# Optimization experiments

Hardware: AMD Instinct MI355X
Metric: run time of the kernel (lower is better)

## Reference

```python
import jax, jax.numpy as jnp
import numpy as np

ORDER = 3  # polynomial filter order


def _sketch_conv(x, A, W, b, coeffs):
    # z = A @ (x W + b); out = sum_d coeffs[d-1] * z**d  (Horner-free power accumulation)
    z = A @ (x @ W + b)            # [N, out_c]
    p = z
    acc = coeffs[0] * z
    for d in range(1, ORDER):      # small fixed loop over polynomial order
        p = p * z
        acc = acc + coeffs[d] * p
    return acc


def setup_inputs() -> dict:
    key = jax.random.key(0)
    ks = jax.random.split(key, 12)
    N, C_IN, C_H, C_OUT = 8192, 128, 64, 40
    nf_mats = jax.random.normal(ks[0], (N, C_IN), dtype=jnp.float32)
    # scale by 1/sqrt(N) so polynomial powers stay O(1)
    conv_mats = jax.random.normal(ks[1], (N, N), dtype=jnp.float32) / np.float32(np.sqrt(N))
    def lin(k, fi, fo):
        kw, kb = jax.random.split(k)
        W = jax.random.normal(kw, (fi, fo), dtype=jnp.float32) / np.float32(np.sqrt(fi))
        b = jax.random.normal(kb, (fo,), dtype=jnp.float32) * np.float32(0.01)
        return W, b
    W1, b1 = lin(ks[2], C_IN, C_H)
    W2, b2 = lin(ks[3], C_H, C_H)
    W3, b3 = lin(ks[4], C_H, C_OUT)
    base = jnp.array([1.0, 0.0, 0.0], dtype=jnp.float32)
    c1 = base + jax.random.normal(ks[5], (ORDER,), dtype=jnp.float32) * 0.05
    c2 = base + jax.random.normal(ks[6], (ORDER,), dtype=jnp.float32) * 0.05
    c3 = base + jax.random.normal(ks[7], (ORDER,), dtype=jnp.float32) * 0.05
    return {"nf_mats": nf_mats, "conv_mats": conv_mats,
            "W1": W1, "b1": b1, "c1": c1,
            "W2": W2, "b2": b2, "c2": c2,
            "W3": W3, "b3": b3, "c3": c3}


def reference(nf_mats, conv_mats, W1, b1, c1, W2, b2, c2, W3, b3, c3):
    # SketchGCN eval-mode forward: batchnorm=False, dropout inactive.
    x = _sketch_conv(nf_mats, conv_mats, W1, b1, c1)      # first layer
    x = x + _sketch_conv(x, conv_mats, W2, b2, c2)        # residual middle layer
    return _sketch_conv(x, conv_mats, W3, b3, c3)         # output layer
```

## Files before the change

kernel.cpp:

```cpp
#include <hip/hip_runtime.h>
#include <stdint.h>

typedef __bf16 bf16x8 __attribute__((ext_vector_type(8)));
typedef float f32x4 __attribute__((ext_vector_type(4)));

using gvoid = const __attribute__((address_space(1))) void;
using lvoid = __attribute__((address_space(3))) void;

__device__ __forceinline__ unsigned short f2bf(float f) {
    union { float f; unsigned u; } x; x.f = f;
    unsigned u = x.u;
    u += 0x7FFFu + ((u >> 16) & 1u);
    return (unsigned short)(u >> 16);
}
__device__ __forceinline__ unsigned pack2(float lo, float hi) {
    return ((unsigned)f2bf(hi) << 16) | (unsigned)f2bf(lo);
}

__global__ __launch_bounds__(256) void convert_bf16(const float* __restrict__ in,
                                                    unsigned short* __restrict__ out,
                                                    int n8) {
    int idx = blockIdx.x * 256 + threadIdx.x;
    int stride = gridDim.x * 256;
    const float4* in4 = (const float4*)in;
    uint4* out8 = (uint4*)out;
    for (int i = idx; i < n8; i += stride) {
        float4 a = in4[2 * i], b = in4[2 * i + 1];
        uint4 o;
        o.x = pack2(a.x, a.y);
        o.y = pack2(a.z, a.w);
        o.z = pack2(b.x, b.y);
        o.w = pack2(b.z, b.w);
        out8[i] = o;
    }
}

template <int CIN>
__global__ __launch_bounds__(256) void small_gemm(const float* __restrict__ X,
                                                  const float* __restrict__ W,
                                                  const float* __restrict__ b,
                                                  int cout,
                                                  unsigned short* __restrict__ Yt) {
    __shared__ float Xs[32 * (CIN + 1)];
    __shared__ float Ws[CIN * 64];
    __shared__ float bs[64];
    const int t = threadIdx.x;
    const int i0 = blockIdx.x * 32;

    for (int e = t; e < 32 * CIN; e += 256) {
        int r = e / CIN, c = e % CIN;
        Xs[r * (CIN + 1) + c] = X[(size_t)(i0 + r) * CIN + c];
    }
    for (int e = t; e < CIN * 64; e += 256) {
        int k = e >> 6, j = e & 63;
        Ws[e] = (j < cout) ? W[k * cout + j] : 0.0f;
    }
    if (t < 64) bs[t] = (t < cout) ? b[t] : 0.0f;
    __syncthreads();

    const int i = t & 31;
    const int jg = t >> 5;
    float acc[8];
#pragma unroll
    for (int jj = 0; jj < 8; ++jj) acc[jj] = 0.0f;

    for (int k = 0; k < CIN; ++k) {
        float xv = Xs[i * (CIN + 1) + k];
        const float4* wr = (const float4*)&Ws[k * 64 + jg * 8];
        float4 w0 = wr[0], w1 = wr[1];
        acc[0] += xv * w0.x; acc[1] += xv * w0.y;
        acc[2] += xv * w0.z; acc[3] += xv * w0.w;
        acc[4] += xv * w1.x; acc[5] += xv * w1.y;
        acc[6] += xv * w1.z; acc[7] += xv * w1.w;
    }
#pragma unroll
    for (int jj = 0; jj < 8; ++jj) {
        int j = jg * 8 + jj;
        Yt[(size_t)j * 8192 + i0 + i] = f2bf(acc[jj] + bs[j]);
    }
}

__global__ __launch_bounds__(256, 4)
void big_gemm(const unsigned short* __restrict__ Ab,
              const unsigned short* __restrict__ Yt,
              float* __restrict__ P) {
    __shared__ unsigned short As[2][64 * 64];
    __shared__ unsigned short Bs[2][64 * 64];
    const int t = threadIdx.x;
    const int lane = t & 63, wid = t >> 6;
    const int lane15 = lane & 15, lane4 = lane >> 4;
    const int wm = wid >> 1, wn = wid & 1;
    const int row0 = blockIdx.x * 64;
    const int kbase = blockIdx.y * 1024;

    f32x4 acc[2][2];
    const f32x4 z4 = {0.f, 0.f, 0.f, 0.f};
#pragma unroll
    for (int m = 0; m < 2; ++m)
#pragma unroll
        for (int n = 0; n < 2; ++n) acc[m][n] = z4;

    auto stage = [&](int nb, int kt) {
#pragma unroll
        for (int ii = 0; ii < 2; ++ii) {
            int p = ii * 256 + wid * 64 + lane;
            int r = p >> 3;
            int c = (p & 7) ^ (r & 7);
            const unsigned short* gp = Ab + (size_t)(row0 + r) * 8192 + (kt + c * 8);
            unsigned short* lp = &As[nb][(ii * 256 + wid * 64) * 8];
            __builtin_amdgcn_global_load_lds((gvoid*)gp, (lvoid*)lp, 16, 0, 0);
        }
#pragma unroll
        for (int ii = 0; ii < 2; ++ii) {
            int q = ii * 256 + wid * 64 + lane;
            int n = q >> 3;
            int c = (q & 7) ^ (n & 7);
            const unsigned short* gp = Yt + (size_t)n * 8192 + (kt + c * 8);
            unsigned short* lp = &Bs[nb][(ii * 256 + wid * 64) * 8];
            __builtin_amdgcn_global_load_lds((gvoid*)gp, (lvoid*)lp, 16, 0, 0);
        }
    };

    stage(0, kbase);
    int buf = 0;
    for (int tt = 0; tt < 16; ++tt) {
        if (tt + 1 < 16) {
            stage(buf ^ 1, kbase + (tt + 1) * 64);
            asm volatile("s_waitcnt vmcnt(4)\n\ts_barrier" ::: "memory");
        } else {
            asm volatile("s_waitcnt vmcnt(0)\n\ts_barrier" ::: "memory");
        }
#pragma unroll
        for (int ks = 0; ks < 2; ++ks) {
            bf16x8 af[2], bfr[2];
#pragma unroll
            for (int m = 0; m < 2; ++m) {
                int r = wm * 32 + m * 16 + lane15;
                int c = ks * 4 + lane4;
                af[m] = *(const bf16x8*)&As[buf][((r << 3) | (c ^ (r & 7))) << 3];
            }
#pragma unroll
            for (int n = 0; n < 2; ++n) {
                int rn = wn * 32 + n * 16 + lane15;
                int c = ks * 4 + lane4;
                bfr[n] = *(const bf16x8*)&Bs[buf][((rn << 3) | (c ^ (rn & 7))) << 3];
            }
#pragma unroll
            for (int m = 0; m < 2; ++m)
#pragma unroll
                for (int n = 0; n < 2; ++n)
                    acc[m][n] = __builtin_amdgcn_mfma_f32_16x16x32_bf16(
                        af[m], bfr[n], acc[m][n], 0, 0, 0);
        }
        asm volatile("s_barrier" ::: "memory");
        buf ^= 1;
    }

    float* Po = P + (size_t)blockIdx.y * (8192 * 64);
#pragma unroll
    for (int m = 0; m < 2; ++m) {
        int r = row0 + wm * 32 + m * 16 + lane4 * 4;
#pragma unroll
        for (int n = 0; n < 2; ++n) {
            int cc = wn * 32 + n * 16 + lane15;
#pragma unroll
            for (int q = 0; q < 4; ++q)
                Po[(size_t)(r + q) * 64 + cc] = acc[m][n][q];
        }
    }
}

template <int MODE>
__global__ __launch_bounds__(256) void fused_reduce(const float* __restrict__ P,
                                                    const float* __restrict__ cf,
                                                    const float* __restrict__ Wn,
                                                    const float* __restrict__ bn,
                                                    int cout,
                                                    float* __restrict__ X1,
                                                    unsigned short* __restrict__ Yt) {
    __shared__ float Xs[64 * 33];
    __shared__ float Ws[64 * 64];
    __shared__ float bs[64];
    const int t = threadIdx.x;
    const int i0 = blockIdx.x * 32;
    const int NT4 = 8192 * 64 / 4;
    const float4* P4 = (const float4*)P;
    float4* X14 = (float4*)X1;

    for (int e = t; e < 64 * 64; e += 256) {
        int k = e >> 6, j = e & 63;
        Ws[e] = (j < cout) ? Wn[k * cout + j] : 0.0f;
    }
    if (t < 64) bs[t] = (t < cout) ? bn[t] : 0.0f;
    const float c0 = cf[0], c1 = cf[1], c2 = cf[2];

#pragma unroll
    for (int s = 0; s < 2; ++s) {
        int e4 = s * 256 + t;
        int i = e4 >> 4, jc = e4 & 15;
        int base4 = (i0 + i) * 16 + jc;
        float4 z = {0.f, 0.f, 0.f, 0.f};
#pragma unroll
        for (int ks = 0; ks < 8; ++ks) {
            float4 p = P4[(size_t)ks * NT4 + base4];
            z.x += p.x; z.y += p.y; z.z += p.z; z.w += p.w;
        }
        float4 v;
        v.x = z.x * (c0 + z.x * (c1 + z.x * c2));
        v.y = z.y * (c0 + z.y * (c1 + z.y * c2));
        v.z = z.z * (c0 + z.z * (c1 + z.z * c2));
        v.w = z.w * (c0 + z.w * (c1 + z.w * c2));
        if (MODE == 0) {
            X14[base4] = v;
        } else {
            float4 xr = X14[base4];
            v.x += xr.x; v.y += xr.y; v.z += xr.z; v.w += xr.w;
        }
        Xs[(jc * 4 + 0) * 33 + i] = v.x;
        Xs[(jc * 4 + 1) * 33 + i] = v.y;
        Xs[(jc * 4 + 2) * 33 + i] = v.z;
        Xs[(jc * 4 + 3) * 33 + i] = v.w;
    }
    __syncthreads();

    const int i = t & 31;
    const int jg = t >> 5;
    float acc[8];
#pragma unroll
    for (int jj = 0; jj < 8; ++jj) acc[jj] = 0.0f;
    for (int k = 0; k < 64; ++k) {
        float xv = Xs[k * 33 + i];
        const float4* wr = (const float4*)&Ws[k * 64 + jg * 8];
        float4 w0 = wr[0], w1 = wr[1];
        acc[0] += xv * w0.x; acc[1] += xv * w0.y;
        acc[2] += xv * w0.z; acc[3] += xv * w0.w;
        acc[4] += xv * w1.x; acc[5] += xv * w1.y;
        acc[6] += xv * w1.z; acc[7] += xv * w1.w;
    }
#pragma unroll
    for (int jj = 0; jj < 8; ++jj) {
        int j = jg * 8 + jj;
        Yt[(size_t)j * 8192 + i0 + i] = f2bf(acc[jj] + bs[j]);
    }
}

__global__ void reduce_out(const float* __restrict__ P, const float* __restrict__ cf,
                           float* __restrict__ out) {
    int e4 = blockIdx.x * 256 + threadIdx.x;
    const int NT4 = 8192 * 64 / 4;
    const float4* P4 = (const float4*)P;
    float4 z = {0.f, 0.f, 0.f, 0.f};
#pragma unroll
    for (int ks = 0; ks < 8; ++ks) {
        float4 p = P4[(size_t)ks * NT4 + e4];
        z.x += p.x; z.y += p.y; z.z += p.z; z.w += p.w;
    }
    float c0 = cf[0], c1 = cf[1], c2 = cf[2];
    float4 v;
    v.x = z.x * (c0 + z.x * (c1 + z.x * c2));
    v.y = z.y * (c0 + z.y * (c1 + z.y * c2));
    v.z = z.z * (c0 + z.z * (c1 + z.z * c2));
    v.w = z.w * (c0 + z.w * (c1 + z.w * c2));
    int i = e4 >> 4, jc = e4 & 15;
    if (jc < 10) ((float4*)out)[i * 10 + jc] = v;
}

extern "C" void kernel_launch(void* const* d_in, const int* in_sizes, int n_in,
                              void* d_out, int out_size, void* d_ws, size_t ws_size,
                              hipStream_t stream) {
    const float* nf   = (const float*)d_in[0];
    const float* Amat = (const float*)d_in[1];
    const float* W1   = (const float*)d_in[2];
    const float* b1   = (const float*)d_in[3];
    const float* c1   = (const float*)d_in[4];
    const float* W2   = (const float*)d_in[5];
    const float* b2   = (const float*)d_in[6];
    const float* c2   = (const float*)d_in[7];
    const float* W3   = (const float*)d_in[8];
    const float* b3   = (const float*)d_in[9];
    const float* c3   = (const float*)d_in[10];
    float* out = (float*)d_out;

    char* ws = (char*)d_ws;
    unsigned short* Abf = (unsigned short*)(ws);
    unsigned short* Yt  = (unsigned short*)(ws + 134217728);
    float* X1           = (float*)(ws + 135266304);
    float* Pp           = (float*)(ws + 137363456);

    convert_bf16<<<2048, 256, 0, stream>>>(Amat, Abf, 8192 * 8192 / 8);
    small_gemm<128><<<256, 256, 0, stream>>>(nf, W1, b1, 64, Yt);

    big_gemm<<<dim3(128, 8), 256, 0, stream>>>(Abf, Yt, Pp);
    fused_reduce<0><<<256, 256, 0, stream>>>(Pp, c1, W2, b2, 64, X1, Yt);

    big_gemm<<<dim3(128, 8), 256, 0, stream>>>(Abf, Yt, Pp);
    fused_reduce<1><<<256, 256, 0, stream>>>(Pp, c2, W3, b3, 40, X1, Yt);

    big_gemm<<<dim3(128, 8), 256, 0, stream>>>(Abf, Yt, Pp);
    reduce_out<<<512, 256, 0, stream>>>(Pp, c3, out);
}
```

Baseline: 204.0 us.

## Replace LDS staging in big GEMM with direct register prefetch pipeline

```diff
diff --git a/kernel.cpp b/kernel.cpp
--- a/kernel.cpp
+++ b/kernel.cpp
@@ -3,9 +3,6 @@
 
 typedef __bf16 bf16x8 __attribute__((ext_vector_type(8)));
 typedef float f32x4 __attribute__((ext_vector_type(4)));
-
-using gvoid = const __attribute__((address_space(1))) void;
-using lvoid = __attribute__((address_space(3))) void;
 
 __device__ __forceinline__ unsigned short f2bf(float f) {
     union { float f; unsigned u; } x; x.f = f;
@@ -80,12 +77,10 @@
     }
 }
 
-__global__ __launch_bounds__(256, 4)
+__global__ __launch_bounds__(256)
 void big_gemm(const unsigned short* __restrict__ Ab,
               const unsigned short* __restrict__ Yt,
               float* __restrict__ P) {
-    __shared__ unsigned short As[2][64 * 64];
-    __shared__ unsigned short Bs[2][64 * 64];
     const int t = threadIdx.x;
     const int lane = t & 63, wid = t >> 6;
     const int lane15 = lane & 15, lane4 = lane >> 4;
@@ -93,6 +88,21 @@
     const int row0 = blockIdx.x * 64;
     const int kbase = blockIdx.y * 1024;
 
+    const unsigned short* aP[2][2];
+    const unsigned short* bP[2][2];
+#pragma unroll
+    for (int m = 0; m < 2; ++m)
+#pragma unroll
+        for (int ks = 0; ks < 2; ++ks)
+            aP[m][ks] = Ab + (size_t)(row0 + wm * 32 + m * 16 + lane15) * 8192 +
+                        kbase + ks * 32 + lane4 * 8;
+#pragma unroll
+    for (int n = 0; n < 2; ++n)
+#pragma unroll
+        for (int ks = 0; ks < 2; ++ks)
+            bP[n][ks] = Yt + (size_t)(wn * 32 + n * 16 + lane15) * 8192 +
+                        kbase + ks * 32 + lane4 * 8;
+
     f32x4 acc[2][2];
     const f32x4 z4 = {0.f, 0.f, 0.f, 0.f};
 #pragma unroll
@@ -100,60 +110,40 @@
 #pragma unroll
         for (int n = 0; n < 2; ++n) acc[m][n] = z4;
 
-    auto stage = [&](int nb, int kt) {
-#pragma unroll
-        for (int ii = 0; ii < 2; ++ii) {
-            int p = ii * 256 + wid * 64 + lane;
-            int r = p >> 3;
-            int c = (p & 7) ^ (r & 7);
-            const unsigned short* gp = Ab + (size_t)(row0 + r) * 8192 + (kt + c * 8);
-            unsigned short* lp = &As[nb][(ii * 256 + wid * 64) * 8];
-            __builtin_amdgcn_global_load_lds((gvoid*)gp, (lvoid*)lp, 16, 0, 0);
-        }
-#pragma unroll
-        for (int ii = 0; ii < 2; ++ii) {
-            int q = ii * 256 + wid * 64 + lane;
-            int n = q >> 3;
-            int c = (q & 7) ^ (n & 7);
-            const unsigned short* gp = Yt + (size_t)n * 8192 + (kt + c * 8);
-            unsigned short* lp = &Bs[nb][(ii * 256 + wid * 64) * 8];
-            __builtin_amdgcn_global_load_lds((gvoid*)gp, (lvoid*)lp, 16, 0, 0);
-        }
+    bf16x8 a[3][2][2];
+    bf16x8 b[2][2][2];
+
+    auto loadA = [&](int d, int tt) {
+#pragma unroll
+        for (int m = 0; m < 2; ++m)
+#pragma unroll
+            for (int ks = 0; ks < 2; ++ks)
+                a[d][m][ks] = *(const bf16x8*)(aP[m][ks] + tt * 64);
     };
-
-    stage(0, kbase);
-    int buf = 0;
+    auto loadB = [&](int d, int tt) {
+#pragma unroll
+        for (int n = 0; n < 2; ++n)
+#pragma unroll
+            for (int ks = 0; ks < 2; ++ks)
+                b[d][n][ks] = *(const bf16x8*)(bP[n][ks] + tt * 64);
+    };
+
+    loadA(0, 0); loadA(1, 1); loadA(2, 2);
+    loadB(0, 0); loadB(1, 1);
+
+#pragma unroll
     for (int tt = 0; tt < 16; ++tt) {
-        if (tt + 1 < 16) {
-            stage(buf ^ 1, kbase + (tt + 1) * 64);
-            asm volatile("s_waitcnt vmcnt(4)\n\ts_barrier" ::: "memory");
-        } else {
-            asm volatile("s_waitcnt vmcnt(0)\n\ts_barrier" ::: "memory");
-        }
-#pragma unroll
-        for (int ks = 0; ks < 2; ++ks) {
-            bf16x8 af[2], bfr[2];
-#pragma unroll
-            for (int m = 0; m < 2; ++m) {
-                int r = wm * 32 + m * 16 + lane15;
-                int c = ks * 4 + lane4;
-                af[m] = *(const bf16x8*)&As[buf][((r << 3) | (c ^ (r & 7))) << 3];
-            }
-#pragma unroll
-            for (int n = 0; n < 2; ++n) {
-                int rn = wn * 32 + n * 16 + lane15;
-                int c = ks * 4 + lane4;
-                bfr[n] = *(const bf16x8*)&Bs[buf][((rn << 3) | (c ^ (rn & 7))) << 3];
-            }
+        const int ad = tt % 3, bd = tt % 2;
+#pragma unroll
+        for (int ks = 0; ks < 2; ++ks)
 #pragma unroll
             for (int m = 0; m < 2; ++m)
 #pragma unroll
                 for (int n = 0; n < 2; ++n)
                     acc[m][n] = __builtin_amdgcn_mfma_f32_16x16x32_bf16(
-                        af[m], bfr[n], acc[m][n], 0, 0, 0);
-        }
-        asm volatile("s_barrier" ::: "memory");
-        buf ^= 1;
+                        a[ad][m][ks], b[bd][n][ks], acc[m][n], 0, 0, 0);
+        if (tt + 3 < 16) loadA(ad, tt + 3);
+        if (tt + 2 < 16) loadB(bd, tt + 2);
     }
 
     float* Po = P + (size_t)blockIdx.y * (8192 * 64);
```

Result: slower. 313.8 us (+53.8%).

## Fuse big GEMM with epilogue, drop split-K partials, deepen LDS pipeline

Applied to the files above, without the earlier changes.

```diff
diff --git a/kernel.cpp b/kernel.cpp
--- a/kernel.cpp
+++ b/kernel.cpp
@@ -80,34 +80,54 @@
     }
 }
 
-__global__ __launch_bounds__(256, 4)
-void big_gemm(const unsigned short* __restrict__ Ab,
-              const unsigned short* __restrict__ Yt,
-              float* __restrict__ P) {
-    __shared__ unsigned short As[2][64 * 64];
-    __shared__ unsigned short Bs[2][64 * 64];
+#define STEPW(N) asm volatile("s_waitcnt vmcnt(" #N ")\n\ts_barrier" ::: "memory")
+#define ENDB()   asm volatile("s_barrier" ::: "memory")
+
+template <int MODE>
+__global__ __launch_bounds__(256)
+void gemm_fused(const unsigned short* __restrict__ Ab,
+                const unsigned short* __restrict__ Ytin,
+                float* __restrict__ X1,
+                const float* __restrict__ Wn,
+                const float* __restrict__ bn,
+                const float* __restrict__ cf,
+                int cout,
+                unsigned short* __restrict__ Ytout,
+                float* __restrict__ out) {
+    __shared__ unsigned short As[8][32 * 64];
+    __shared__ unsigned short Bs[8][64 * 64];
+    __shared__ float Ws[64 * 64];
+    __shared__ float bs[64];
+    __shared__ float Xs[32 * 65];
+
     const int t = threadIdx.x;
     const int lane = t & 63, wid = t >> 6;
     const int lane15 = lane & 15, lane4 = lane >> 4;
     const int wm = wid >> 1, wn = wid & 1;
-    const int row0 = blockIdx.x * 64;
-    const int kbase = blockIdx.y * 1024;
-
-    f32x4 acc[2][2];
-    const f32x4 z4 = {0.f, 0.f, 0.f, 0.f};
-#pragma unroll
-    for (int m = 0; m < 2; ++m)
-#pragma unroll
-        for (int n = 0; n < 2; ++n) acc[m][n] = z4;
-
-    auto stage = [&](int nb, int kt) {
-#pragma unroll
-        for (int ii = 0; ii < 2; ++ii) {
-            int p = ii * 256 + wid * 64 + lane;
+    const int row0 = blockIdx.x * 32;
+
+    if constexpr (MODE < 2) {
+        for (int e = t; e < 64 * 64; e += 256) {
+            int k = e >> 6, j = e & 63;
+            Ws[e] = (j < cout) ? Wn[k * cout + j] : 0.0f;
+        }
+        if (t < 64) bs[t] = (t < cout) ? bn[t] : 0.0f;
+    }
+    asm volatile("s_waitcnt vmcnt(0)" ::: "memory");
+
+    f32x4 acc[2];
+    acc[0] = (f32x4){0.f, 0.f, 0.f, 0.f};
+    acc[1] = (f32x4){0.f, 0.f, 0.f, 0.f};
+
+    auto stage = [&](int tile) {
+        const int nb = tile & 7;
+        const int kt = tile * 64;
+        {
+            int p = wid * 64 + lane;
             int r = p >> 3;
             int c = (p & 7) ^ (r & 7);
             const unsigned short* gp = Ab + (size_t)(row0 + r) * 8192 + (kt + c * 8);
-            unsigned short* lp = &As[nb][(ii * 256 + wid * 64) * 8];
+            unsigned short* lp = &As[nb][(wid * 64) * 8];
             __builtin_amdgcn_global_load_lds((gvoid*)gp, (lvoid*)lp, 16, 0, 0);
         }
 #pragma unroll
@@ -115,154 +135,93 @@
             int q = ii * 256 + wid * 64 + lane;
             int n = q >> 3;
             int c = (q & 7) ^ (n & 7);
-            const unsigned short* gp = Yt + (size_t)n * 8192 + (kt + c * 8);
+            const unsigned short* gp = Ytin + (size_t)n * 8192 + (kt + c * 8);
             unsigned short* lp = &Bs[nb][(ii * 256 + wid * 64) * 8];
             __builtin_amdgcn_global_load_lds((gvoid*)gp, (lvoid*)lp, 16, 0, 0);
         }
     };
 
-    stage(0, kbase);
-    int buf = 0;
-    for (int tt = 0; tt < 16; ++tt) {
-        if (tt + 1 < 16) {
-            stage(buf ^ 1, kbase + (tt + 1) * 64);
-            asm volatile("s_waitcnt vmcnt(4)\n\ts_barrier" ::: "memory");
-        } else {
-            asm volatile("s_waitcnt vmcnt(0)\n\ts_barrier" ::: "memory");
-        }
+    auto compute = [&](int tile) {
+        const int b7 = tile & 7;
 #pragma unroll
         for (int ks = 0; ks < 2; ++ks) {
-            bf16x8 af[2], bfr[2];
-#pragma unroll
-            for (int m = 0; m < 2; ++m) {
-                int r = wm * 32 + m * 16 + lane15;
+            bf16x8 af, bfr[2];
+            {
+                int r = wm * 16 + lane15;
                 int c = ks * 4 + lane4;
-                af[m] = *(const bf16x8*)&As[buf][((r << 3) | (c ^ (r & 7))) << 3];
+                af = *(const bf16x8*)&As[b7][((r << 3) | (c ^ (r & 7))) << 3];
             }
 #pragma unroll
             for (int n = 0; n < 2; ++n) {
                 int rn = wn * 32 + n * 16 + lane15;
                 int c = ks * 4 + lane4;
-                bfr[n] = *(const bf16x8*)&Bs[buf][((rn << 3) | (c ^ (rn & 7))) << 3];
+                bfr[n] = *(const bf16x8*)&Bs[b7][((rn << 3) | (c ^ (rn & 7))) << 3];
             }
 #pragma unroll
-            for (int m = 0; m < 2; ++m)
-#pragma unroll
-                for (int n = 0; n < 2; ++n)
-                    acc[m][n] = __builtin_amdgcn_mfma_f32_16x16x32_bf16(
-                        af[m], bfr[n], acc[m][n], 0, 0, 0);
-        }
-        asm volatile("s_barrier" ::: "memory");
-        buf ^= 1;
-    }
-
-    float* Po = P + (size_t)blockIdx.y * (8192 * 64);
-#pragma unroll
-    for (int m = 0; m < 2; ++m) {
-        int r = row0 + wm * 32 + m * 16 + lane4 * 4;
-#pragma unroll
-        for (int n = 0; n < 2; ++n) {
-            int cc = wn * 32 + n * 16 + lane15;
-#pragma unroll
-            for (int q = 0; q < 4; ++q)
-                Po[(size_t)(r + q) * 64 + cc] = acc[m][n][q];
-        }
-    }
-}
-
-template <int MODE>
-__global__ __launch_bounds__(256) void fused_reduce(const float* __restrict__ P,
-                                                    const float* __restrict__ cf,
-                                                    const float* __restrict__ Wn,
-                                                    const float* __restrict__ bn,
-                                                    int cout,
-                                                    float* __restrict__ X1,
-                                                    unsigned short* __restrict__ Yt) {
-    __shared__ float Xs[64 * 33];
-    __shared__ float Ws[64 * 64];
-    __shared__ float bs[64];
-    const int t = threadIdx.x;
-    const int i0 = blockIdx.x * 32;
-    const int NT4 = 8192 * 64 / 4;
-    const float4* P4 = (const float4*)P;
-    float4* X14 = (float4*)X1;
-
-    for (int e = t; e < 64 * 64; e += 256) {
-        int k = e >> 6, j = e & 63;
-        Ws[e] = (j < cout) ? Wn[k * cout + j] : 0.0f;
-    }
-    if (t < 64) bs[t] = (t < cout) ? bn[t] : 0.0f;
+            for (int n = 0; n < 2; ++n)
+                acc[n] = __builtin_amdgcn_mfma_f32_16x16x32_bf16(af, bfr[n], acc[n], 0, 0, 0);
+        }
+    };
+
+#pragma unroll
+    for (int i = 0; i < 6; ++i) stage(i);
+
+    for (int tt = 0; tt < 128; ++tt) {
+        if (tt < 122)      { stage(tt + 6); STEPW(18); }
+        else if (tt == 122) STEPW(15);
+        else if (tt == 123) STEPW(12);
+        else if (tt == 124) STEPW(9);
+        else if (tt == 125) STEPW(6);
+        else if (tt == 126) STEPW(3);
+        else                STEPW(0);
+        compute(tt);
+        ENDB();
+    }
+
     const float c0 = cf[0], c1 = cf[1], c2 = cf[2];
-
-#pragma unroll
-    for (int s = 0; s < 2; ++s) {
-        int e4 = s * 256 + t;
-        int i = e4 >> 4, jc = e4 & 15;
-        int base4 = (i0 + i) * 16 + jc;
-        float4 z = {0.f, 0.f, 0.f, 0.f};
-#pragma unroll
-        for (int ks = 0; ks < 8; ++ks) {
-            float4 p = P4[(size_t)ks * NT4 + base4];
-            z.x += p.x; z.y += p.y; z.z += p.z; z.w += p.w;
-        }
-        float4 v;
-        v.x = z.x * (c0 + z.x * (c1 + z.x * c2));
-        v.y = z.y * (c0 + z.y * (c1 + z.y * c2));
-        v.z = z.z * (c0 + z.z * (c1 + z.z * c2));
-        v.w = z.w * (c0 + z.w * (c1 + z.w * c2));
-        if (MODE == 0) {
-            X14[base4] = v;
-        } else {
-            float4 xr = X14[base4];
-            v.x += xr.x; v.y += xr.y; v.z += xr.z; v.w += xr.w;
-        }
-        Xs[(jc * 4 + 0) * 33 + i] = v.x;
-        Xs[(jc * 4 + 1) * 33 + i] = v.y;
-        Xs[(jc * 4 + 2) * 33 + i] = v.z;
-        Xs[(jc * 4 + 3) * 33 + i] = v.w;
-    }
+    const int rloc = wm * 16 + lane4 * 4;
+#pragma unroll
+    for (int n = 0; n < 2; ++n) {
+        const int cc = wn * 32 + n * 16 + lane15;
+#pragma unroll
+        for (int q = 0; q < 4; ++q) {
+            float z = acc[n][q];
+            float v = z * (c0 + z * (c1 + z * c2));
+            const int gi = row0 + rloc + q;
+            if constexpr (MODE == 0) {
+                X1[(size_t)gi * 64 + cc] = v;
+                Xs[(rloc + q) * 65 + cc] = v;
+            } else if constexpr (MODE == 1) {
+                v += X1[(size_t)gi * 64 + cc];
+                Xs[(rloc + q) * 65 + cc] = v;
+            } else {
+                if (cc < 40) out[(size_t)gi * 40 + cc] = v;
+            }
+        }
+    }
+    if constexpr (MODE == 2) return;
+
     __syncthreads();
 
     const int i = t & 31;
     const int jg = t >> 5;
-    float acc[8];
-#pragma unroll
-    for (int jj = 0; jj < 8; ++jj) acc[jj] = 0.0f;
+    float a8[8];
+#pragma unroll
+    for (int jj = 0; jj < 8; ++jj) a8[jj] = 0.0f;
     for (int k = 0; k < 64; ++k) {
-        float xv = Xs[k * 33 + i];
+        float xv = Xs[i * 65 + k];
         const float4* wr = (const float4*)&Ws[k * 64 + jg * 8];
         float4 w0 = wr[0], w1 = wr[1];
-        acc[0] += xv * w0.x; acc[1] += xv * w0.y;
-        acc[2] += xv * w0.z; acc[3] += xv * w0.w;
-        acc[4] += xv * w1.x; acc[5] += xv * w1.y;
-        acc[6] += xv * w1.z; acc[7] += xv * w1.w;
+        a8[0] += xv * w0.x; a8[1] += xv * w0.y;
+        a8[2] += xv * w0.z; a8[3] += xv * w0.w;
+        a8[4] += xv * w1.x; a8[5] += xv * w1.y;
+        a8[6] += xv * w1.z; a8[7] += xv * w1.w;
     }
 #pragma unroll
     for (int jj = 0; jj < 8; ++jj) {
         int j = jg * 8 + jj;
-        Yt[(size_t)j * 8192 + i0 + i] = f2bf(acc[jj] + bs[j]);
-    }
-}
-
-__global__ void reduce_out(const float* __restrict__ P, const float* __restrict__ cf,
-                           float* __restrict__ out) {
-    int e4 = blockIdx.x * 256 + threadIdx.x;
-    const int NT4 = 8192 * 64 / 4;
-    const float4* P4 = (const float4*)P;
-    float4 z = {0.f, 0.f, 0.f, 0.f};
-#pragma unroll
-    for (int ks = 0; ks < 8; ++ks) {
-        float4 p = P4[(size_t)ks * NT4 + e4];
-        z.x += p.x; z.y += p.y; z.z += p.z; z.w += p.w;
-    }
-    float c0 = cf[0], c1 = cf[1], c2 = cf[2];
-    float4 v;
-    v.x = z.x * (c0 + z.x * (c1 + z.x * c2));
-    v.y = z.y * (c0 + z.y * (c1 + z.y * c2));
-    v.z = z.z * (c0 + z.z * (c1 + z.z * c2));
-    v.w = z.w * (c0 + z.w * (c1 + z.w * c2));
-    int i = e4 >> 4, jc = e4 & 15;
-    if (jc < 10) ((float4*)out)[i * 10 + jc] = v;
+        Ytout[(size_t)j * 8192 + row0 + i] = f2bf(a8[jj] + bs[j]);
+    }
 }
 
 extern "C" void kernel_launch(void* const* d_in, const int* in_sizes, int n_in,
@@ -283,19 +242,15 @@
 
     char* ws = (char*)d_ws;
     unsigned short* Abf = (unsigned short*)(ws);
-    unsigned short* Yt  = (unsigned short*)(ws + 134217728);
-    float* X1           = (float*)(ws + 135266304);
-    float* Pp           = (float*)(ws + 137363456);
+    unsigned short* YtA = (unsigned short*)(ws + 134217728);
+    unsigned short* YtB = (unsigned short*)(ws + 135266304);
+    float* X1           = (float*)(ws + 136314880);
 
     convert_bf16<<<2048, 256, 0, stream>>>(Amat, Abf, 8192 * 8192 / 8);
-    small_gemm<128><<<256, 256, 0, stream>>>(nf, W1, b1, 64, Yt);
-
-    big_gemm<<<dim3(128, 8), 256, 0, stream>>>(Abf, Yt, Pp);
-    fused_reduce<0><<<256, 256, 0, stream>>>(Pp, c1, W2, b2, 64, X1, Yt);
-
-    big_gemm<<<dim3(128, 8), 256, 0, stream>>>(Abf, Yt, Pp);
-    fused_reduce<1><<<256, 256, 0, stream>>>(Pp, c2, W3, b3, 40, X1, Yt);
-
-    big_gemm<<<dim3(128, 8), 256, 0, stream>>>(Abf, Yt, Pp);
-    reduce_out<<<512, 256, 0, stream>>>(Pp, c3, out);
-}
+    small_gemm<128><<<256, 256, 0, stream>>>(nf, W1, b1, 64, YtA);
+
+    gemm_fused<0><<<256, 256, 0, stream>>>(Abf, YtA, X1, W2, b2, c1, 64, YtB, nullptr);
+    gemm_fused<1><<<256, 256, 0, stream>>>(Abf, YtB, X1, W3, b3, c2, 40, YtA, nullptr);
+    gemm_fused<2><<<256, 256, 0, stream>>>(Abf, YtA, nullptr, nullptr, nullptr, c3, 0,
+                                           nullptr, out);
+}
```

Result: slower. 343.6 us (+68.4%).

## Load B operand straight to registers and fuse conversion with first small GEMM

Applied to the files above, without the earlier changes.

```diff
diff --git a/kernel.cpp b/kernel.cpp
--- a/kernel.cpp
+++ b/kernel.cpp
@@ -17,45 +17,39 @@
     return ((unsigned)f2bf(hi) << 16) | (unsigned)f2bf(lo);
 }
 
-__global__ __launch_bounds__(256) void convert_bf16(const float* __restrict__ in,
-                                                    unsigned short* __restrict__ out,
-                                                    int n8) {
-    int idx = blockIdx.x * 256 + threadIdx.x;
-    int stride = gridDim.x * 256;
-    const float4* in4 = (const float4*)in;
-    uint4* out8 = (uint4*)out;
-    for (int i = idx; i < n8; i += stride) {
-        float4 a = in4[2 * i], b = in4[2 * i + 1];
-        uint4 o;
-        o.x = pack2(a.x, a.y);
-        o.y = pack2(a.z, a.w);
-        o.z = pack2(b.x, b.y);
-        o.w = pack2(b.z, b.w);
-        out8[i] = o;
-    }
-}
-
-template <int CIN>
-__global__ __launch_bounds__(256) void small_gemm(const float* __restrict__ X,
-                                                  const float* __restrict__ W,
-                                                  const float* __restrict__ b,
-                                                  int cout,
-                                                  unsigned short* __restrict__ Yt) {
-    __shared__ float Xs[32 * (CIN + 1)];
-    __shared__ float Ws[CIN * 64];
+__global__ __launch_bounds__(256)
+void convert_small(const float* __restrict__ Amat, unsigned short* __restrict__ Abf,
+                   const float* __restrict__ X, const float* __restrict__ W,
+                   const float* __restrict__ b, unsigned short* __restrict__ Yt) {
+    __shared__ float Xs[32 * 129];
+    __shared__ float Ws[128 * 64];
     __shared__ float bs[64];
     const int t = threadIdx.x;
-    const int i0 = blockIdx.x * 32;
-
-    for (int e = t; e < 32 * CIN; e += 256) {
-        int r = e / CIN, c = e % CIN;
-        Xs[r * (CIN + 1) + c] = X[(size_t)(i0 + r) * CIN + c];
-    }
-    for (int e = t; e < CIN * 64; e += 256) {
-        int k = e >> 6, j = e & 63;
-        Ws[e] = (j < cout) ? W[k * cout + j] : 0.0f;
-    }
-    if (t < 64) bs[t] = (t < cout) ? b[t] : 0.0f;
+
+    if (blockIdx.x < 2048) {
+        const int n8 = 8192 * 8192 / 8;
+        int idx = blockIdx.x * 256 + t;
+        const float4* in4 = (const float4*)Amat;
+        uint4* out8 = (uint4*)Abf;
+        for (int i = idx; i < n8; i += 2048 * 256) {
+            float4 a = in4[2 * i], c = in4[2 * i + 1];
+            uint4 o;
+            o.x = pack2(a.x, a.y);
+            o.y = pack2(a.z, a.w);
+            o.z = pack2(c.x, c.y);
+            o.w = pack2(c.z, c.w);
+            out8[i] = o;
+        }
+        return;
+    }
+
+    const int i0 = (blockIdx.x - 2048) * 32;
+    for (int e = t; e < 32 * 128; e += 256) {
+        int r = e >> 7, c = e & 127;
+        Xs[r * 129 + c] = X[(size_t)(i0 + r) * 128 + c];
+    }
+    for (int e = t; e < 128 * 64; e += 256) Ws[e] = W[e];
+    if (t < 64) bs[t] = b[t];
     __syncthreads();
 
     const int i = t & 31;
@@ -63,9 +57,8 @@
     float acc[8];
 #pragma unroll
     for (int jj = 0; jj < 8; ++jj) acc[jj] = 0.0f;
-
-    for (int k = 0; k < CIN; ++k) {
-        float xv = Xs[i * (CIN + 1) + k];
+    for (int k = 0; k < 128; ++k) {
+        float xv = Xs[i * 129 + k];
         const float4* wr = (const float4*)&Ws[k * 64 + jg * 8];
         float4 w0 = wr[0], w1 = wr[1];
         acc[0] += xv * w0.x; acc[1] += xv * w0.y;
@@ -85,7 +78,6 @@
               const unsigned short* __restrict__ Yt,
               float* __restrict__ P) {
     __shared__ unsigned short As[2][64 * 64];
-    __shared__ unsigned short Bs[2][64 * 64];
     const int t = threadIdx.x;
     const int lane = t & 63, wid = t >> 6;
     const int lane15 = lane & 15, lane4 = lane >> 4;
@@ -93,6 +85,14 @@
     const int row0 = blockIdx.x * 64;
     const int kbase = blockIdx.y * 1024;
 
+    const unsigned short* bP[2][2];
+#pragma unroll
+    for (int n = 0; n < 2; ++n)
+#pragma unroll
+        for (int ks = 0; ks < 2; ++ks)
+            bP[n][ks] = Yt + (size_t)(wn * 32 + n * 16 + lane15) * 8192 +
+                        kbase + ks * 32 + lane4 * 8;
+
     f32x4 acc[2][2];
     const f32x4 z4 = {0.f, 0.f, 0.f, 0.f};
 #pragma unroll
@@ -100,60 +100,58 @@
 #pragma unroll
         for (int n = 0; n < 2; ++n) acc[m][n] = z4;
 
-    auto stage = [&](int nb, int kt) {
+    bf16x8 breg[2][2][2];
+
+    auto stageA = [&](int slot, int kt) {
 #pragma unroll
         for (int ii = 0; ii < 2; ++ii) {
             int p = ii * 256 + wid * 64 + lane;
             int r = p >> 3;
             int c = (p & 7) ^ (r & 7);
             const unsigned short* gp = Ab + (size_t)(row0 + r) * 8192 + (kt + c * 8);
-            unsigned short* lp = &As[nb][(ii * 256 + wid * 64) * 8];
+            unsigned short* lp = &As[slot][(ii * 256 + wid * 64) * 8];
             __builtin_amdgcn_global_load_lds((gvoid*)gp, (lvoid*)lp, 16, 0, 0);
         }
-#pragma unroll
-        for (int ii = 0; ii < 2; ++ii) {
-            int q = ii * 256 + wid * 64 + lane;
-            int n = q >> 3;
-            int c = (q & 7) ^ (n & 7);
-            const unsigned short* gp = Yt + (size_t)n * 8192 + (kt + c * 8);
-            unsigned short* lp = &Bs[nb][(ii * 256 + wid * 64) * 8];
-            __builtin_amdgcn_global_load_lds((gvoid*)gp, (lvoid*)lp, 16, 0, 0);
-        }
     };
 
-    stage(0, kbase);
-    int buf = 0;
+    stageA(0, kbase);
+#pragma unroll
+    for (int n = 0; n < 2; ++n)
+#pragma unroll
+        for (int ks = 0; ks < 2; ++ks)
+            breg[0][n][ks] = *(const bf16x8*)(bP[n][ks]);
+
+#pragma unroll
     for (int tt = 0; tt < 16; ++tt) {
         if (tt + 1 < 16) {
-            stage(buf ^ 1, kbase + (tt + 1) * 64);
-            asm volatile("s_waitcnt vmcnt(4)\n\ts_barrier" ::: "memory");
+            stageA((tt + 1) & 1, kbase + (tt + 1) * 64);
+#pragma unroll
+            for (int n = 0; n < 2; ++n)
+#pragma unroll
+                for (int ks = 0; ks < 2; ++ks)
+                    breg[(tt + 1) & 1][n][ks] =
+                        *(const bf16x8*)(bP[n][ks] + (tt + 1) * 64);
+            asm volatile("s_waitcnt vmcnt(6)\n\ts_barrier" ::: "memory");
         } else {
             asm volatile("s_waitcnt vmcnt(0)\n\ts_barrier" ::: "memory");
         }
 #pragma unroll
         for (int ks = 0; ks < 2; ++ks) {
-            bf16x8 af[2], bfr[2];
+            bf16x8 af[2];
 #pragma unroll
             for (int m = 0; m < 2; ++m) {
                 int r = wm * 32 + m * 16 + lane15;
                 int c = ks * 4 + lane4;
-                af[m] = *(const bf16x8*)&As[buf][((r << 3) | (c ^ (r & 7))) << 3];
-            }
-#pragma unroll
-            for (int n = 0; n < 2; ++n) {
-                int rn = wn * 32 + n * 16 + lane15;
-                int c = ks * 4 + lane4;
-                bfr[n] = *(const bf16x8*)&Bs[buf][((rn << 3) | (c ^ (rn & 7))) << 3];
+                af[m] = *(const bf16x8*)&As[tt & 1][((r << 3) | (c ^ (r & 7))) << 3];
             }
 #pragma unroll
             for (int m = 0; m < 2; ++m)
 #pragma unroll
                 for (int n = 0; n < 2; ++n)
                     acc[m][n] = __builtin_amdgcn_mfma_f32_16x16x32_bf16(
-                        af[m], bfr[n], acc[m][n], 0, 0, 0);
+                        af[m], breg[tt & 1][n][ks], acc[m][n], 0, 0, 0);
         }
         asm volatile("s_barrier" ::: "memory");
-        buf ^= 1;
     }
 
     float* Po = P + (size_t)blockIdx.y * (8192 * 64);
@@ -287,8 +285,7 @@
     float* X1           = (float*)(ws + 135266304);
     float* Pp           = (float*)(ws + 137363456);
 
-    convert_bf16<<<2048, 256, 0, stream>>>(Amat, Abf, 8192 * 8192 / 8);
-    small_gemm<128><<<256, 256, 0, stream>>>(nf, W1, b1, 64, Yt);
+    convert_small<<<2304, 256, 0, stream>>>(Amat, Abf, nf, W1, b1, Yt);
 
     big_gemm<<<dim3(128, 8), 256, 0, stream>>>(Abf, Yt, Pp);
     fused_reduce<0><<<256, 256, 0, stream>>>(Pp, c1, W2, b2, 64, X1, Yt);
```

Result: slower. 236.2 us (+15.8%).
